# Optimization experiments

Hardware: AMD Instinct MI355X
Metric: run time of the kernel (lower is better)

## Reference

```python
import jax, jax.numpy as jnp
import numpy as np

TEMP = 0.07
NEG_INF = -1e30  # finite stand-in for -inf; safe under vjp


def setup_inputs() -> dict:
    key = jax.random.key(0)
    k1, k2, k3 = jax.random.split(key, 3)
    B, D, H, F = 16384, 2048, 2048, 128  # 2N rows, backbone_dim, hidden_dim, feature_dim
    features = jax.random.normal(k1, (B, D), dtype=jnp.float32)
    w1 = jax.random.normal(k2, (D, H), dtype=jnp.float32) / np.sqrt(D)
    b1 = jnp.zeros((H,), dtype=jnp.float32)
    w2 = jax.random.normal(k3, (H, F), dtype=jnp.float32) / np.sqrt(H)
    b2 = jnp.zeros((F,), dtype=jnp.float32)
    return {"features": features, "w1": w1, "b1": b1, "w2": w2, "b2": b2}


def reference(features, w1, b1, w2, b2):
    # Projector: Linear -> ReLU -> Linear, then L2-normalize (F.normalize, dim=1)
    h = jax.nn.relu(features @ w1 + b1)
    p = h @ w2 + b2
    z = p / jnp.maximum(jnp.linalg.norm(p, axis=1, keepdims=True), 1e-12)

    M = z.shape[0]           # 2N
    N = M // 2
    sim = (z @ z.T) / TEMP   # [2N, 2N]

    # NT-Xent with labels=0: loss_i = logsumexp_{j != i}(sim[i,j]) - pos_i
    # (pos appears exactly once among the logits, so the gather loop over
    #  per-row negatives collapses to a diagonal-masked row logsumexp).
    diag = jnp.eye(M, dtype=bool)
    lse = jax.nn.logsumexp(jnp.where(diag, NEG_INF, sim), axis=1)
    pos = jnp.sum(z * jnp.roll(z, N, axis=0), axis=1) / TEMP  # sim[i, (i+N) % 2N]
    loss = jnp.mean(lse - pos)
    return loss, z[:N], z[N:]
```

## Files before the change

### kernel.cpp

```cpp
#include <hip/hip_runtime.h>

typedef __attribute__((ext_vector_type(8))) __bf16 bf16x8;
typedef __attribute__((ext_vector_type(4))) float f32x4;

#define B_ROWS 16384
#define N_HALF 8192
#define D_DIM  2048
#define H_DIM  2048
#define F_DIM  128

static constexpr float kInvT = 14.285714285714286f;
static constexpr float kS2   = 20.60992915555662f;

__device__ __forceinline__ void async16(void* lds, const void* g) {
  __builtin_amdgcn_global_load_lds((const __attribute__((address_space(1))) void*)g,
                                   (__attribute__((address_space(3))) void*)lds,
                                   16, 0, 0);
}

__global__ void cvt_bf16_kernel(const float* __restrict__ in, __bf16* __restrict__ out, int n) {
  int i = (blockIdx.x * blockDim.x + threadIdx.x) * 8;
  if (i >= n) return;
  float4 a = *(const float4*)(in + i);
  float4 b = *(const float4*)(in + i + 4);
  bf16x8 o;
  o[0] = (__bf16)a.x; o[1] = (__bf16)a.y; o[2] = (__bf16)a.z; o[3] = (__bf16)a.w;
  o[4] = (__bf16)b.x; o[5] = (__bf16)b.y; o[6] = (__bf16)b.z; o[7] = (__bf16)b.w;
  *(bf16x8*)(out + i) = o;
}

__global__ void transpose_cvt_kernel(const float* __restrict__ in, __bf16* __restrict__ out,
                                     int R, int C) {
  __shared__ float tile[32][33];
  int tx = threadIdx.x, ty = threadIdx.y;
  int c0 = blockIdx.x * 32, r0 = blockIdx.y * 32;
  for (int i = 0; i < 4; i++)
    tile[ty + i * 8][tx] = in[(size_t)(r0 + ty + i * 8) * C + c0 + tx];
  __syncthreads();
  for (int i = 0; i < 4; i++)
    out[(size_t)(c0 + ty + i * 8) * R + r0 + tx] = (__bf16)tile[tx][ty + i * 8];
}

#define BM 256
#define BK 64
#define NT_K (D_DIM / BK)

__global__ __launch_bounds__(512, 2) void gemm1_8ph_kernel(
    const __bf16* __restrict__ A, const __bf16* __restrict__ BT,
    const float* __restrict__ bias, __bf16* __restrict__ C) {
  __shared__ __align__(16) __bf16 As[2][BM * BK];
  __shared__ __align__(16) __bf16 Bs[2][BM * BK];
  const int t = threadIdx.x;
  const int wave = t >> 6, lane = t & 63;
  const int l15 = lane & 15, quad = lane >> 4, l7 = l15 & 7;
  const int wy = wave & 1, wx = wave >> 1;

  const int wg = ((int)blockIdx.x & 7) * 64 + ((int)blockIdx.x >> 3);
  const int n0 = (wg & 7) * 256;
  const int m0 = (wg >> 3) * 256;

  const int tr = t >> 3;
  const int csw = ((t & 7) ^ (tr & 7)) * 8;
  const __bf16* pA = A + (size_t)(m0 + tr) * D_DIM + csw;
  const __bf16* pB = BT + (size_t)(n0 + tr) * D_DIM + csw;
  const int ldsw = wave * 512;

  auto stageA = [&](int buf, int h, int kk) {
    async16(&As[buf][h * 8192 + ldsw], pA + (size_t)(h * 128) * D_DIM + kk);
    async16(&As[buf][h * 8192 + 4096 + ldsw], pA + (size_t)(h * 128 + 64) * D_DIM + kk);
  };
  auto stageB = [&](int buf, int h, int kk) {
    async16(&Bs[buf][h * 8192 + ldsw], pB + (size_t)(h * 128) * D_DIM + kk);
    async16(&Bs[buf][h * 8192 + 4096 + ldsw], pB + (size_t)(h * 128 + 64) * D_DIM + kk);
  };

  const int arow = wy * 16 + l15;
  const int brow = wx * 16 + l15;
  const int s0 = (quad ^ l7) * 8;
  const int s1 = ((4 + quad) ^ l7) * 8;

  f32x4 acc[8][4];
#pragma unroll
  for (int f = 0; f < 8; f++)
#pragma unroll
    for (int n = 0; n < 4; n++) acc[f][n] = 0.f;

  stageB(0, 0, 0); stageB(0, 1, 0);
  stageA(0, 0, 0); stageA(0, 1, 0);
  stageB(1, 0, BK); stageB(1, 1, BK);
  asm volatile("s_waitcnt vmcnt(4)" ::: "memory");
  __builtin_amdgcn_s_barrier();

  for (int tk = 0; tk < NT_K; ++tk) {
    const int cur = tk & 1, nxt = cur ^ 1;
    const __bf16* Ac = &As[cur][0];
    const __bf16* Bc = &Bs[cur][0];
#define LDA(f, s) (*(const bf16x8*)(Ac + ((f) * 32 + arow) * 64 + (s)))
#define LDB(n, s) (*(const bf16x8*)(Bc + ((n) * 64 + brow) * 64 + (s)))
    bf16x8 b0[4], b1[4];
    {
      bf16x8 a0 = LDA(0, s0), a1 = LDA(1, s0), a2 = LDA(2, s0), a3 = LDA(3, s0);
      b0[0] = LDB(0, s0); b0[1] = LDB(1, s0); b0[2] = LDB(2, s0); b0[3] = LDB(3, s0);
      if (tk + 1 < NT_K) stageA(nxt, 0, (tk + 1) * BK);
      __builtin_amdgcn_s_barrier();
      asm volatile("s_waitcnt lgkmcnt(0)" ::: "memory");
      __builtin_amdgcn_s_setprio(1);
#pragma unroll
      for (int n = 0; n < 4; n++) {
        acc[0][n] = __builtin_amdgcn_mfma_f32_16x16x32_bf16(a0, b0[n], acc[0][n], 0, 0, 0);
        acc[1][n] = __builtin_amdgcn_mfma_f32_16x16x32_bf16(a1, b0[n], acc[1][n], 0, 0, 0);
        acc[2][n] = __builtin_amdgcn_mfma_f32_16x16x32_bf16(a2, b0[n], acc[2][n], 0, 0, 0);
        acc[3][n] = __builtin_amdgcn_mfma_f32_16x16x32_bf16(a3, b0[n], acc[3][n], 0, 0, 0);
      }
      __builtin_amdgcn_s_setprio(0);
      __builtin_amdgcn_s_barrier();
    }
    {
      bf16x8 a4 = LDA(4, s0), a5 = LDA(5, s0), a6 = LDA(6, s0), a7 = LDA(7, s0);
      if (tk + 1 < NT_K) stageA(nxt, 1, (tk + 1) * BK);
      __builtin_amdgcn_s_barrier();
      asm volatile("s_waitcnt lgkmcnt(0)" ::: "memory");
      __builtin_amdgcn_s_setprio(1);
#pragma unroll
      for (int n = 0; n < 4; n++) {
        acc[4][n] = __builtin_amdgcn_mfma_f32_16x16x32_bf16(a4, b0[n], acc[4][n], 0, 0, 0);
        acc[5][n] = __builtin_amdgcn_mfma_f32_16x16x32_bf16(a5, b0[n], acc[5][n], 0, 0, 0);
        acc[6][n] = __builtin_amdgcn_mfma_f32_16x16x32_bf16(a6, b0[n], acc[6][n], 0, 0, 0);
        acc[7][n] = __builtin_amdgcn_mfma_f32_16x16x32_bf16(a7, b0[n], acc[7][n], 0, 0, 0);
      }
      __builtin_amdgcn_s_setprio(0);
      __builtin_amdgcn_s_barrier();
    }
    {
      bf16x8 a0 = LDA(0, s1), a1 = LDA(1, s1), a2 = LDA(2, s1), a3 = LDA(3, s1);
      b1[0] = LDB(0, s1); b1[1] = LDB(1, s1); b1[2] = LDB(2, s1); b1[3] = LDB(3, s1);
      __builtin_amdgcn_s_barrier();
      asm volatile("s_waitcnt lgkmcnt(0)" ::: "memory");
      __builtin_amdgcn_s_setprio(1);
#pragma unroll
      for (int n = 0; n < 4; n++) {
        acc[0][n] = __builtin_amdgcn_mfma_f32_16x16x32_bf16(a0, b1[n], acc[0][n], 0, 0, 0);
        acc[1][n] = __builtin_amdgcn_mfma_f32_16x16x32_bf16(a1, b1[n], acc[1][n], 0, 0, 0);
        acc[2][n] = __builtin_amdgcn_mfma_f32_16x16x32_bf16(a2, b1[n], acc[2][n], 0, 0, 0);
        acc[3][n] = __builtin_amdgcn_mfma_f32_16x16x32_bf16(a3, b1[n], acc[3][n], 0, 0, 0);
      }
      __builtin_amdgcn_s_setprio(0);
      __builtin_amdgcn_s_barrier();
    }
    {
      bf16x8 a4 = LDA(4, s1), a5 = LDA(5, s1), a6 = LDA(6, s1), a7 = LDA(7, s1);
      if (tk + 2 < NT_K) {
        stageB(cur, 0, (tk + 2) * BK);
        stageB(cur, 1, (tk + 2) * BK);
        asm volatile("s_waitcnt vmcnt(4)" ::: "memory");
      } else if (tk + 1 < NT_K) {
        asm volatile("s_waitcnt vmcnt(0)" ::: "memory");
      }
      __builtin_amdgcn_s_barrier();
      asm volatile("s_waitcnt lgkmcnt(0)" ::: "memory");
      __builtin_amdgcn_s_setprio(1);
#pragma unroll
      for (int n = 0; n < 4; n++) {
        acc[4][n] = __builtin_amdgcn_mfma_f32_16x16x32_bf16(a4, b1[n], acc[4][n], 0, 0, 0);
        acc[5][n] = __builtin_amdgcn_mfma_f32_16x16x32_bf16(a5, b1[n], acc[5][n], 0, 0, 0);
        acc[6][n] = __builtin_amdgcn_mfma_f32_16x16x32_bf16(a6, b1[n], acc[6][n], 0, 0, 0);
        acc[7][n] = __builtin_amdgcn_mfma_f32_16x16x32_bf16(a7, b1[n], acc[7][n], 0, 0, 0);
      }
      __builtin_amdgcn_s_setprio(0);
      __builtin_amdgcn_s_barrier();
    }
#undef LDA
#undef LDB
  }

#pragma unroll
  for (int n = 0; n < 4; n++) {
    int col = n0 + n * 64 + wx * 16 + l15;
    float bv = bias[col];
#pragma unroll
    for (int f = 0; f < 8; f++) {
      int rowb = m0 + f * 32 + wy * 16 + quad * 4;
#pragma unroll
      for (int r = 0; r < 4; r++) {
        float v = fmaxf(acc[f][n][r] + bv, 0.f);
        C[(size_t)(rowb + r) * H_DIM + col] = (__bf16)v;
      }
    }
  }
}

__global__ __launch_bounds__(256) void proj_norm_kernel(
    const __bf16* __restrict__ A, const __bf16* __restrict__ BT,
    const float* __restrict__ bias, float* __restrict__ zf, __bf16* __restrict__ zb, int K) {
  __shared__ __align__(16) __bf16 As[64 * 32];
  __shared__ __align__(16) __bf16 Bs[128 * 32];
  __shared__ float pbuf[64 * 128];
  const int t = threadIdx.x;
  const int wave = t >> 6, lane = t & 63;
  const int l15 = lane & 15, quad = lane >> 4;
  const int wy = wave >> 1, wx = wave & 1;
  const int m0 = blockIdx.x * 64;
  const int sr = t >> 2;
  const int sk = (((t & 3) ^ ((sr >> 1) & 3))) * 8;
  const int sw = (l15 >> 1) & 3;

  f32x4 acc[2][4];
  for (int i = 0; i < 2; i++)
    for (int j = 0; j < 4; j++) acc[i][j] = 0.f;

  for (int k0 = 0; k0 < K; k0 += 32) {
    async16(As + wave * 512, A + (size_t)(m0 + sr) * K + k0 + sk);
    async16(Bs + 0 * 2048 + wave * 512, BT + (size_t)(0  + sr) * K + k0 + sk);
    async16(Bs + 1 * 2048 + wave * 512, BT + (size_t)(64 + sr) * K + k0 + sk);
    __syncthreads();
    bf16x8 af[2], bfr[4];
    for (int i = 0; i < 2; i++)
      af[i] = *(const bf16x8*)(As + (wy * 32 + i * 16 + l15) * 32 + (quad ^ sw) * 8);
    for (int i = 0; i < 4; i++)
      bfr[i] = *(const bf16x8*)(Bs + (wx * 64 + i * 16 + l15) * 32 + (quad ^ sw) * 8);
    for (int mi = 0; mi < 2; mi++)
      for (int ni = 0; ni < 4; ni++)
        acc[mi][ni] = __builtin_amdgcn_mfma_f32_16x16x32_bf16(af[mi], bfr[ni], acc[mi][ni], 0, 0, 0);
    __syncthreads();
  }
  for (int ni = 0; ni < 4; ni++) {
    int col = wx * 64 + ni * 16 + l15;
    float bv = bias[col];
    for (int mi = 0; mi < 2; mi++) {
      int lrow = wy * 32 + mi * 16 + quad * 4;
      for (int r = 0; r < 4; r++)
        pbuf[(lrow + r) * 128 + col] = acc[mi][ni][r] + bv;
    }
  }
  __syncthreads();
  for (int it = 0; it < 16; it++) {
    int lrow = wave * 16 + it;
    float v0 = pbuf[lrow * 128 + lane];
    float v1 = pbuf[lrow * 128 + 64 + lane];
    float ss = v0 * v0 + v1 * v1;
    for (int m = 1; m < 64; m <<= 1) ss += __shfl_xor(ss, m);
    float inv = 1.f / fmaxf(sqrtf(ss), 1e-12f);
    float z0 = v0 * inv, z1 = v1 * inv;
    size_t base = (size_t)(m0 + lrow) * F_DIM;
    zf[base + lane] = z0;
    zf[base + 64 + lane] = z1;
    zb[base + lane] = (__bf16)z0;
    zb[base + 64 + lane] = (__bf16)z1;
  }
}

__global__ __launch_bounds__(256) void sim_lse_kernel(const __bf16* __restrict__ zb,
                                                      float* __restrict__ S) {
  __shared__ __align__(16) __bf16 Bs[128 * 128];
  const int t = threadIdx.x;
  const int wave = t >> 6, lane = t & 63;
  const int l15 = lane & 15, quad = lane >> 4;
  const int wy = wave >> 1, wx = wave & 1;
  const int r0 = blockIdx.y * 128;
  const int c0 = blockIdx.x * 2048;
  const int srow = t >> 4;
  const int schunk = (t & 15) ^ srow;

  bf16x8 a[4][4];
  for (int mi = 0; mi < 4; mi++)
    for (int ks = 0; ks < 4; ks++)
      a[mi][ks] = *(const bf16x8*)(zb + (size_t)(r0 + wy * 64 + mi * 16 + l15) * 128 + ks * 32 + quad * 8);

  float rowacc[4][4];
  for (int mi = 0; mi < 4; mi++)
    for (int r = 0; r < 4; r++) rowacc[mi][r] = 0.f;

  for (int ct = 0; ct < 16; ct++) {
    const __bf16* gbase = zb + (size_t)(c0 + ct * 128) * 128;
    for (int q = 0; q < 8; q++)
      async16(Bs + q * 2048 + wave * 512, gbase + (size_t)(q * 16 + srow) * 128 + schunk * 8);
    __syncthreads();
    const bool diag_tile = (c0 + ct * 128 == r0);
    for (int ni = 0; ni < 4; ni++) {
      bf16x8 b[4];
      const int brow = wx * 64 + ni * 16 + l15;
      for (int ks = 0; ks < 4; ks++)
        b[ks] = *(const bf16x8*)(Bs + brow * 128 + (((ks * 4 + quad) ^ l15) * 8));
      for (int mi = 0; mi < 4; mi++) {
        f32x4 acc = 0.f;
        for (int ks = 0; ks < 4; ks++)
          acc = __builtin_amdgcn_mfma_f32_16x16x32_bf16(a[mi][ks], b[ks], acc, 0, 0, 0);
        if (diag_tile) {
          int j = c0 + ct * 128 + brow;
          int ibase = r0 + wy * 64 + mi * 16 + quad * 4;
          for (int r = 0; r < 4; r++) {
            float term = __builtin_amdgcn_exp2f(fmaf(acc[r], kS2, -kS2));
            rowacc[mi][r] += (ibase + r == j) ? 0.f : term;
          }
        } else {
          for (int r = 0; r < 4; r++)
            rowacc[mi][r] += __builtin_amdgcn_exp2f(fmaf(acc[r], kS2, -kS2));
        }
      }
    }
    __syncthreads();
  }
  for (int mi = 0; mi < 4; mi++)
    for (int r = 0; r < 4; r++) {
      float v = rowacc[mi][r];
      v += __shfl_xor(v, 1);
      v += __shfl_xor(v, 2);
      v += __shfl_xor(v, 4);
      v += __shfl_xor(v, 8);
      if (l15 == 0)
        atomicAdd(&S[r0 + wy * 64 + mi * 16 + quad * 4 + r], v);
    }
}

__global__ void loss_kernel(const float* __restrict__ zf, const float* __restrict__ S,
                            float* __restrict__ out) {
  int wave = threadIdx.x >> 6, lane = threadIdx.x & 63;
  int base = blockIdx.x * 64 + wave * 16;
  float local = 0.f;
  for (int it = 0; it < 16; it++) {
    int row = base + it;
    int j = (row + N_HALF) & (B_ROWS - 1);
    const float* za = zf + (size_t)row * F_DIM;
    const float* zc = zf + (size_t)j * F_DIM;
    float d = za[lane] * zc[lane] + za[lane + 64] * zc[lane + 64];
    for (int m = 1; m < 64; m <<= 1) d += __shfl_xor(d, m);
    float pos = d * kInvT;
    float lse = logf(S[row]) + kInvT;
    local += (lse - pos);
  }
  if (lane == 0) atomicAdd(out, local * (1.f / B_ROWS));
}

extern "C" void kernel_launch(void* const* d_in, const int* in_sizes, int n_in,
                              void* d_out, int out_size, void* d_ws, size_t ws_size,
                              hipStream_t stream) {
  const float* features = (const float*)d_in[0];
  const float* w1 = (const float*)d_in[1];
  const float* b1 = (const float*)d_in[2];
  const float* w2 = (const float*)d_in[3];
  const float* b2 = (const float*)d_in[4];
  float* out = (float*)d_out;

  char* ws = (char*)d_ws;
  size_t off = 0;
  __bf16* A1  = (__bf16*)(ws + off); off += (size_t)B_ROWS * D_DIM * 2;
  __bf16* h   = (__bf16*)(ws + off); off += (size_t)B_ROWS * H_DIM * 2;
  __bf16* w1t = (__bf16*)(ws + off); off += (size_t)H_DIM * D_DIM * 2;
  __bf16* w2t = (__bf16*)(ws + off); off += (size_t)F_DIM * H_DIM * 2;
  __bf16* zbb = (__bf16*)(ws + off); off += (size_t)B_ROWS * F_DIM * 2;
  float*  S   = (float*)(ws + off);  off += (size_t)B_ROWS * 4;

  hipMemsetAsync(S, 0, (size_t)B_ROWS * 4, stream);
  hipMemsetAsync(out, 0, 4, stream);

  {
    int n = B_ROWS * D_DIM;
    cvt_bf16_kernel<<<n / (256 * 8), 256, 0, stream>>>(features, A1, n);
  }
  transpose_cvt_kernel<<<dim3(H_DIM / 32, D_DIM / 32), dim3(32, 8), 0, stream>>>(w1, w1t, D_DIM, H_DIM);
  transpose_cvt_kernel<<<dim3(F_DIM / 32, H_DIM / 32), dim3(32, 8), 0, stream>>>(w2, w2t, H_DIM, F_DIM);

  gemm1_8ph_kernel<<<dim3((B_ROWS / 256) * (H_DIM / 256)), 512, 0, stream>>>(A1, w1t, b1, h);

  proj_norm_kernel<<<B_ROWS / 64, 256, 0, stream>>>(h, w2t, b2, out + 1, zbb, H_DIM);

  sim_lse_kernel<<<dim3(8, B_ROWS / 128), 256, 0, stream>>>(zbb, S);

  loss_kernel<<<B_ROWS / 64, 256, 0, stream>>>(out + 1, S, out);
}
```

Baseline: 487.3 us.

## Exploit symmetry of similarity matrix with triangular tile schedule

Replaces the full 2D tiling of the z·zᵀ logsumexp kernel with a linearized upper-triangular tile schedule. Each block handles 8 consecutive tiles and maps its index to a (row, col) tile pair. Off-diagonal tiles add their exp terms to both the row sums and the column sums through extra atomics, so each pair is computed once. This roughly halves the MFMA and exp work, at the cost of more atomic traffic and some imbalance around row-tile switches.

```diff
diff --git a/kernel.cpp b/kernel.cpp
--- a/kernel.cpp
+++ b/kernel.cpp
@@ -249,67 +249,116 @@
   }
 }
 
-__global__ __launch_bounds__(256) void sim_lse_kernel(const __bf16* __restrict__ zb,
-                                                      float* __restrict__ S) {
+__global__ __launch_bounds__(256) void sim_lse_tri_kernel(const __bf16* __restrict__ zb,
+                                                          float* __restrict__ S) {
   __shared__ __align__(16) __bf16 Bs[128 * 128];
   const int t = threadIdx.x;
   const int wave = t >> 6, lane = t & 63;
   const int l15 = lane & 15, quad = lane >> 4;
   const int wy = wave >> 1, wx = wave & 1;
-  const int r0 = blockIdx.y * 128;
-  const int c0 = blockIdx.x * 2048;
   const int srow = t >> 4;
   const int schunk = (t & 15) ^ srow;
 
+  const int u = blockIdx.x * 8;
+  auto fr = [](int r) { return r * 128 - (r * (r - 1)) / 2; };
+  int rt = (int)(128.5f - sqrtf(16512.25f - 2.0f * (float)u));
+  while (fr(rt + 1) <= u) rt++;
+  while (fr(rt) > u) rt--;
+  int ct = rt + (u - fr(rt));
+
   bf16x8 a[4][4];
+  float rowacc[4][4];
+  auto load_a = [&](int rtile) {
+#pragma unroll
+    for (int mi = 0; mi < 4; mi++)
+#pragma unroll
+      for (int ks = 0; ks < 4; ks++)
+        a[mi][ks] = *(const bf16x8*)(zb + (size_t)(rtile * 128 + wy * 64 + mi * 16 + l15) * 128 +
+                                     ks * 32 + quad * 8);
+  };
+  auto flush_rows = [&](int rtile) {
+#pragma unroll
+    for (int mi = 0; mi < 4; mi++)
+#pragma unroll
+      for (int r = 0; r < 4; r++) {
+        float v = rowacc[mi][r];
+        v += __shfl_xor(v, 1);
+        v += __shfl_xor(v, 2);
+        v += __shfl_xor(v, 4);
+        v += __shfl_xor(v, 8);
+        if (l15 == 0)
+          atomicAdd(&S[rtile * 128 + wy * 64 + mi * 16 + quad * 4 + r], v);
+        rowacc[mi][r] = 0.f;
+      }
+  };
+
+#pragma unroll
   for (int mi = 0; mi < 4; mi++)
-    for (int ks = 0; ks < 4; ks++)
-      a[mi][ks] = *(const bf16x8*)(zb + (size_t)(r0 + wy * 64 + mi * 16 + l15) * 128 + ks * 32 + quad * 8);
-
-  float rowacc[4][4];
-  for (int mi = 0; mi < 4; mi++)
+#pragma unroll
     for (int r = 0; r < 4; r++) rowacc[mi][r] = 0.f;
-
-  for (int ct = 0; ct < 16; ct++) {
-    const __bf16* gbase = zb + (size_t)(c0 + ct * 128) * 128;
+  load_a(rt);
+
+  for (int it = 0; it < 8; ++it) {
+    const __bf16* gbase = zb + (size_t)(ct * 128) * 128;
+#pragma unroll
     for (int q = 0; q < 8; q++)
       async16(Bs + q * 2048 + wave * 512, gbase + (size_t)(q * 16 + srow) * 128 + schunk * 8);
     __syncthreads();
-    const bool diag_tile = (c0 + ct * 128 == r0);
+    const bool diag = (ct == rt);
+#pragma unroll
     for (int ni = 0; ni < 4; ni++) {
       bf16x8 b[4];
       const int brow = wx * 64 + ni * 16 + l15;
+#pragma unroll
       for (int ks = 0; ks < 4; ks++)
         b[ks] = *(const bf16x8*)(Bs + brow * 128 + (((ks * 4 + quad) ^ l15) * 8));
-      for (int mi = 0; mi < 4; mi++) {
-        f32x4 acc = 0.f;
-        for (int ks = 0; ks < 4; ks++)
-          acc = __builtin_amdgcn_mfma_f32_16x16x32_bf16(a[mi][ks], b[ks], acc, 0, 0, 0);
-        if (diag_tile) {
-          int j = c0 + ct * 128 + brow;
-          int ibase = r0 + wy * 64 + mi * 16 + quad * 4;
+      float colsum = 0.f;
+      if (diag) {
+#pragma unroll
+        for (int mi = 0; mi < 4; mi++) {
+          f32x4 acc = 0.f;
+#pragma unroll
+          for (int ks = 0; ks < 4; ks++)
+            acc = __builtin_amdgcn_mfma_f32_16x16x32_bf16(a[mi][ks], b[ks], acc, 0, 0, 0);
+          const int lrb = wy * 64 + mi * 16 + quad * 4;
+#pragma unroll
           for (int r = 0; r < 4; r++) {
             float term = __builtin_amdgcn_exp2f(fmaf(acc[r], kS2, -kS2));
-            rowacc[mi][r] += (ibase + r == j) ? 0.f : term;
+            rowacc[mi][r] += (lrb + r == brow) ? 0.f : term;
           }
-        } else {
-          for (int r = 0; r < 4; r++)
-            rowacc[mi][r] += __builtin_amdgcn_exp2f(fmaf(acc[r], kS2, -kS2));
         }
+      } else {
+#pragma unroll
+        for (int mi = 0; mi < 4; mi++) {
+          f32x4 acc = 0.f;
+#pragma unroll
+          for (int ks = 0; ks < 4; ks++)
+            acc = __builtin_amdgcn_mfma_f32_16x16x32_bf16(a[mi][ks], b[ks], acc, 0, 0, 0);
+#pragma unroll
+          for (int r = 0; r < 4; r++) {
+            float term = __builtin_amdgcn_exp2f(fmaf(acc[r], kS2, -kS2));
+            rowacc[mi][r] += term;
+            colsum += term;
+          }
+        }
+        colsum += __shfl_xor(colsum, 16);
+        colsum += __shfl_xor(colsum, 32);
+        if (quad == 0)
+          atomicAdd(&S[ct * 128 + brow], colsum);
       }
     }
     __syncthreads();
-  }
-  for (int mi = 0; mi < 4; mi++)
-    for (int r = 0; r < 4; r++) {
-      float v = rowacc[mi][r];
-      v += __shfl_xor(v, 1);
-      v += __shfl_xor(v, 2);
-      v += __shfl_xor(v, 4);
-      v += __shfl_xor(v, 8);
-      if (l15 == 0)
-        atomicAdd(&S[r0 + wy * 64 + mi * 16 + quad * 4 + r], v);
-    }
+    if (it < 7) {
+      ct++;
+      if (ct == 128) {
+        flush_rows(rt);
+        rt++;
+        ct = rt;
+        load_a(rt);
+      }
+    }
+  }
+  flush_rows(rt);
 }
 
 __global__ void loss_kernel(const float* __restrict__ zf, const float* __restrict__ S,
@@ -364,7 +413,7 @@
 
   proj_norm_kernel<<<B_ROWS / 64, 256, 0, stream>>>(h, w2t, b2, out + 1, zbb, H_DIM);
 
-  sim_lse_kernel<<<dim3(8, B_ROWS / 128), 256, 0, stream>>>(zbb, S);
+  sim_lse_tri_kernel<<<1032, 256, 0, stream>>>(zbb, S);
 
   loss_kernel<<<B_ROWS / 64, 256, 0, stream>>>(out + 1, S, out);
 }
```

Measured after the change: 486.9 us. Within noise of the previous version (-0.1%).
